# Kernel tuning notes

Measured on AMD Instinct MI355X. Metric: run time of the kernel, lower is better.

The kernel has to match this reference:

```python
import jax, jax.numpy as jnp
import numpy as np

D = 1024      # d_model
E = 8         # num_experts
K = 2         # top_k
H = 4096      # expert_dim (bottleneck)
P = 256       # proj_dim
BATCH, SEQ = 2, 2048
CLAMP_MAX = float(np.log(1.0 / 0.01))
INIT_T = 0.5


def setup_inputs() -> dict:
    key = jax.random.key(0)
    ks = jax.random.split(key, 6)
    x = jax.random.normal(ks[0], (BATCH, SEQ, D), jnp.float32)
    # cosine projector (nn.Linear default init ~ U(-1/sqrt(D), 1/sqrt(D)))
    lim = 1.0 / np.sqrt(D)
    Wp = jax.random.uniform(ks[1], (P, D), jnp.float32, -lim, lim)
    bp = jnp.zeros((P,), jnp.float32)
    sim = 0.01 * jax.random.normal(ks[2], (P, E), jnp.float32)
    temp = jnp.full((1,), np.log(1.0 / INIT_T), jnp.float32)
    # RepAdapter 1x1 convs == linear layers; xavier_uniform, zero bias
    bA = float(np.sqrt(6.0 / (D + H)))
    A = jax.random.uniform(ks[3], (E, H, D), jnp.float32, -bA, bA)
    a_bias = jnp.zeros((E, H), jnp.float32)
    Bw = jax.random.uniform(ks[4], (E, D, H), jnp.float32, -bA, bA)
    b_bias = jnp.zeros((E, D), jnp.float32)
    return dict(x=x, Wp=Wp, bp=bp, sim=sim, temp=temp, A=A, a_bias=a_bias, Bw=Bw, b_bias=b_bias)


def reference(x, Wp, bp, sim, temp, A, a_bias, Bw, b_bias):
    B, S, d = x.shape
    e = sim.shape[1]
    xf = x.reshape(-1, d)                                  # [T, D]
    # cosine gate
    proj = xf @ Wp.T + bp                                  # [T, P]
    projn = proj / jnp.maximum(jnp.linalg.norm(proj, axis=1, keepdims=True), 1e-12)
    simn = sim / jnp.maximum(jnp.linalg.norm(sim, axis=0, keepdims=True), 1e-12)
    scale = jnp.exp(jnp.minimum(temp, CLAMP_MAX))          # [1]
    gate_probs = jax.nn.softmax((projn @ simn) * scale, axis=-1)   # [T, E]
    topv, topi = jax.lax.top_k(gate_probs, K)              # [T, K]
    topv = topv / (topv.sum(axis=-1, keepdims=True) + 1e-8)
    # per-token per-expert combine weight
    w = jnp.sum(topv[:, :, None] * jax.nn.one_hot(topi, e, dtype=x.dtype), axis=1)  # [T, E]

    # experts: y_e(x) = x + B_e(A_e x + a_e) + b_e (no nonlinearity); combine weighted
    def body(acc, params):
        Ae, ab, Be, bb, we = params
        h = xf @ Ae.T + ab                                 # [T, H]
        f = h @ Be.T + bb                                  # [T, D]
        return acc + we[:, None] * (xf + f), None

    out, _ = jax.lax.scan(body, jnp.zeros_like(xf), (A, a_bias, Bw, b_bias, w.T))
    out = out.reshape(B, S, d)

    frac = gate_probs.mean(axis=0)                         # expert_fractions
    aux_loss = jnp.sum((frac - 1.0 / e) ** 2)
    usage = jnp.bincount(topi.reshape(-1), length=e).astype(jnp.float32)
    return out, aux_loss, frac, usage
```

## Files before the change

kernel.cpp:

```cpp
#include <hip/hip_runtime.h>
#include <stdint.h>


typedef __attribute__((ext_vector_type(4))) float floatx4;
typedef __attribute__((ext_vector_type(8))) short shortx8;
typedef unsigned short ushort_t;

#define T_TOKENS 4096
#define D_DIM    1024
#define E_EXP    8
#define H_DIM    4096
#define P_DIM    256
#define ROWS_PAD 10240
#define MBLK     40
#define MBLK1    80

__device__ __forceinline__ ushort_t f2bf(float f) {
  union { float f; unsigned int u; } c; c.f = f;
  unsigned int u = c.u;
  unsigned int r = u + 0x7FFFu + ((u >> 16) & 1u);
  return (ushort_t)(r >> 16);
}

__device__ __forceinline__ void stage16(const ushort_t* g, ushort_t* l) {
  __builtin_amdgcn_global_load_lds((const __attribute__((address_space(1))) void*)g,
                                   (__attribute__((address_space(3))) void*)l, 16, 0, 0);
}

__global__ __launch_bounds__(256) void k_cvt2(const float* __restrict__ srcA,
                                              const float* __restrict__ srcB,
                                              ushort_t* __restrict__ dstA,
                                              ushort_t* __restrict__ dstB) {
  int g = blockIdx.x * 256 + threadIdx.x;
  const float* s; ushort_t* d; int i;
  if (g < 8388608) { s = srcA; d = dstA; i = g; }
  else             { s = srcB; d = dstB; i = g - 8388608; }
  floatx4 v = ((const floatx4*)s)[i];
  ushort4 o; o.x = f2bf(v.x); o.y = f2bf(v.y); o.z = f2bf(v.z); o.w = f2bf(v.w);
  ((ushort4*)d)[i] = o;
}

__global__ __launch_bounds__(256) void k_small_init(int* counts, int* cursor,
                                                    float* frac_sum, int* row2tok) {
  int g = blockIdx.x * 256 + threadIdx.x;
  if (g < 8) { counts[g] = 0; cursor[g] = 0; frac_sum[g] = 0.f; }
  if (g < ROWS_PAD) row2tok[g] = -1;
}

__global__ __launch_bounds__(256) void k_proj(const float* __restrict__ x,
                                              const float* __restrict__ Wp,
                                              const float* __restrict__ bp,
                                              float* __restrict__ proj) {
  __shared__ float Wc[256 * 36];
  __shared__ float Xc[16 * 36];
  int tid = threadIdx.x;
  int t0 = blockIdx.x * 16;
  int cg = tid & 31, tg = tid >> 5;
  floatx4 acc[2][8];
#pragma unroll
  for (int a = 0; a < 2; a++)
#pragma unroll
    for (int b = 0; b < 8; b++) acc[a][b] = (floatx4){0.f, 0.f, 0.f, 0.f};
  for (int kc = 0; kc < 32; ++kc) {
    int k0 = kc * 32;
    __syncthreads();
#pragma unroll
    for (int it = 0; it < 8; ++it) {
      int f = it * 256 + tid;
      int j = f >> 3, kk = (f & 7) << 2;
      floatx4 v = *(const floatx4*)(Wp + j * 1024 + k0 + kk);
      *(floatx4*)(Wc + j * 36 + kk) = v;
    }
    if (tid < 128) {
      int t = tid >> 3, kk = (tid & 7) << 2;
      floatx4 v = *(const floatx4*)(x + (size_t)(t0 + t) * 1024 + k0 + kk);
      *(floatx4*)(Xc + t * 36 + kk) = v;
    }
    __syncthreads();
#pragma unroll
    for (int k4 = 0; k4 < 8; ++k4) {
      floatx4 xv[2], wv[8];
#pragma unroll
      for (int tt = 0; tt < 2; tt++) xv[tt] = *(floatx4*)(Xc + (tg * 2 + tt) * 36 + k4 * 4);
#pragma unroll
      for (int jj = 0; jj < 8; jj++) wv[jj] = *(floatx4*)(Wc + (cg + jj * 32) * 36 + k4 * 4);
#pragma unroll
      for (int tt = 0; tt < 2; tt++)
#pragma unroll
        for (int jj = 0; jj < 8; jj++) acc[tt][jj] += xv[tt] * wv[jj];
    }
  }
#pragma unroll
  for (int tt = 0; tt < 2; tt++)
#pragma unroll
    for (int jj = 0; jj < 8; jj++) {
      floatx4 a = acc[tt][jj];
      float s = (a.x + a.y) + (a.z + a.w);
      int t = t0 + tg * 2 + tt, j = cg + jj * 32;
      proj[t * 256 + j] = s + bp[j];
    }
}

__global__ __launch_bounds__(128) void k_gate(const float* __restrict__ proj,
                                              const float* __restrict__ sim,
                                              const float* __restrict__ temp,
                                              int* __restrict__ topi, float* __restrict__ wslot,
                                              float* __restrict__ swsum,
                                              float* __restrict__ frac_sum, int* __restrict__ counts) {
  __shared__ float simT[8][256];
  __shared__ float snorm[8];
  __shared__ float fracs[8];
  __shared__ int cnts[8];
  int tid = threadIdx.x;
  for (int i = tid; i < 2048; i += 128) { int p = i >> 3, e = i & 7; simT[e][p] = sim[i]; }
  if (tid < 8) { fracs[tid] = 0.f; cnts[tid] = 0; }
  __syncthreads();
  if (tid < 8) {
    float s = 0.f;
    for (int p = 0; p < 256; p++) { float v = simT[tid][p]; s += v * v; }
    snorm[tid] = fmaxf(sqrtf(s), 1e-12f);
  }
  __syncthreads();
  int t = blockIdx.x * 128 + tid;
  floatx4 n4 = (floatx4){0.f, 0.f, 0.f, 0.f};
  floatx4 d4[8];
#pragma unroll
  for (int e = 0; e < 8; e++) d4[e] = (floatx4){0.f, 0.f, 0.f, 0.f};
  const floatx4* pr = (const floatx4*)(proj + t * 256);
  for (int k4 = 0; k4 < 64; ++k4) {
    floatx4 p = pr[k4];
    n4 += p * p;
#pragma unroll
    for (int e = 0; e < 8; e++) d4[e] += p * *(const floatx4*)(&simT[e][k4 * 4]);
  }
  float nrm = fmaxf(sqrtf((n4.x + n4.y) + (n4.z + n4.w)), 1e-12f);
  float scale = expf(fminf(temp[0], 4.6051701859880914f));
  float pe[8];
  float mx = -1e30f;
#pragma unroll
  for (int e = 0; e < 8; e++) {
    float d = (d4[e].x + d4[e].y) + (d4[e].z + d4[e].w);
    pe[e] = d / (nrm * snorm[e]) * scale;
    mx = fmaxf(mx, pe[e]);
  }
  float sum = 0.f;
#pragma unroll
  for (int e = 0; e < 8; e++) { pe[e] = expf(pe[e] - mx); sum += pe[e]; }
#pragma unroll
  for (int e = 0; e < 8; e++) pe[e] /= sum;
  int i0 = 0;
#pragma unroll
  for (int e = 1; e < 8; e++) if (pe[e] > pe[i0]) i0 = e;
  int i1 = (i0 == 0) ? 1 : 0;
#pragma unroll
  for (int e = 0; e < 8; e++) if (e != i1 && e != i0 && pe[e] > pe[i1]) i1 = e;
  float v0 = pe[i0], v1 = pe[i1];
  float s2 = v0 + v1 + 1e-8f;
  float w0 = v0 / s2, w1 = v1 / s2;
  topi[t * 2] = i0; topi[t * 2 + 1] = i1;
  wslot[t * 2] = w0; wslot[t * 2 + 1] = w1;
  swsum[t] = w0 + w1;
#pragma unroll
  for (int e = 0; e < 8; e++) atomicAdd(&fracs[e], pe[e]);
  atomicAdd(&cnts[i0], 1); atomicAdd(&cnts[i1], 1);
  __syncthreads();
  if (tid < 8) { atomicAdd(&frac_sum[tid], fracs[tid]); atomicAdd(&counts[tid], cnts[tid]); }
}

__global__ void k_scan(const int* __restrict__ counts, const float* __restrict__ frac_sum,
                       int* __restrict__ offsets, int* __restrict__ blk2e,
                       float* __restrict__ out_tail) {
  __shared__ int offs[9];
  if (threadIdx.x == 0) {
    int off = 0;
    for (int e = 0; e < 8; e++) { offs[e] = off; off += ((counts[e] + 255) >> 8) << 8; }
    offs[8] = off;
    for (int e = 0; e < 9; e++) offsets[e] = offs[e];
    float aux = 0.f;
    for (int e = 0; e < 8; e++) { float fr = frac_sum[e] / 4096.f; aux += (fr - 0.125f) * (fr - 0.125f); }
    out_tail[0] = aux;
  }
  __syncthreads();
  int tid = threadIdx.x;
  if (tid < MBLK) {
    int r = tid * 256, e = -1;
    for (int q = 0; q < 8; q++) if (r >= offs[q] && r < offs[q + 1]) e = q;
    blk2e[tid] = e;
  }
  if (tid < 8) {
    out_tail[1 + tid] = frac_sum[tid] / 4096.f;
    out_tail[9 + tid] = (float)counts[tid];
  }
}

__global__ __launch_bounds__(256) void k_assign(const int* __restrict__ topi,
                                                const float* __restrict__ wslot,
                                                const int* __restrict__ offsets,
                                                int* __restrict__ cursor,
                                                int* __restrict__ row2tok, float* __restrict__ roww) {
  int g = blockIdx.x * 256 + threadIdx.x;
  if (g >= 8192) return;
  int t = g >> 1;
  int e = topi[g];
  int pos = atomicAdd(&cursor[e], 1);
  int r = offsets[e] + pos;
  row2tok[r] = t;
  roww[r] = wslot[g];
}

__global__ __launch_bounds__(256) void k_gather(const float* __restrict__ x,
                                                const int* __restrict__ row2tok,
                                                ushort_t* __restrict__ xg) {
  int r = blockIdx.x * 4 + (threadIdx.x >> 6);
  int l = threadIdx.x & 63;
  int t = row2tok[r];
  ushort4* dst = (ushort4*)(xg + (size_t)r * 1024);
  if (t < 0) {
    ushort4 z; z.x = z.y = z.z = z.w = 0;
    for (int i = l; i < 256; i += 64) dst[i] = z;
  } else {
    const floatx4* src = (const floatx4*)(x + (size_t)t * 1024);
    for (int i = l; i < 256; i += 64) {
      floatx4 v = src[i];
      ushort4 o; o.x = f2bf(v.x); o.y = f2bf(v.y); o.z = f2bf(v.z); o.w = f2bf(v.w);
      dst[i] = o;
    }
  }
}

__global__ __launch_bounds__(256) void k_init_out(const float* __restrict__ x,
                                                  const float* __restrict__ swsum,
                                                  float* __restrict__ out) {
  int g = blockIdx.x * 256 + threadIdx.x;
  float s = swsum[g >> 8];
  floatx4 v = ((const floatx4*)x)[g];
  ((floatx4*)out)[g] = v * s;
}

__global__ __launch_bounds__(256, 2) void k_gemm1(const ushort_t* __restrict__ Aop0,
                                                  const ushort_t* __restrict__ Wall,
                                                  const float* __restrict__ bias,
                                                  const int* __restrict__ blk2e,
                                                  ushort_t* __restrict__ hout) {
  const int K = 1024, N = 4096;
  int gx = gridDim.x;
  int nwg = gx * gridDim.y;
  int flat = blockIdx.y * gx + blockIdx.x;
  int qq = nwg >> 3, rr = nwg & 7;
  int xcd = flat & 7, idx = flat >> 3;
  int swz = (xcd < rr ? xcd * (qq + 1) : rr * (qq + 1) + (xcd - rr) * qq) + idx;
  int rb = swz / gx, nb = swz - rb * gx;
  int e = blk2e[rb >> 1];
  if (e < 0) return;
  const ushort_t* Aop = Aop0 + (size_t)rb * 128 * K;
  const ushort_t* Bop = Wall + (size_t)e * N * K + (size_t)nb * 128 * K;

  __shared__ ushort_t As[2][8192], Bs[2][8192];

  int tid = threadIdx.x, lane = tid & 63, wv = tid >> 6;
  int l15 = lane & 15, q = lane >> 4;
  int wm = (wv & 1) << 6, wn = (wv >> 1) << 6;
  floatx4 acc[4][4];
#pragma unroll
  for (int i = 0; i < 4; i++)
#pragma unroll
    for (int j = 0; j < 4; j++) acc[i][j] = (floatx4){0.f, 0.f, 0.f, 0.f};

  int srow = tid >> 3, schunk = tid & 7;

  auto stage = [&](int kt, int buf) {
#pragma unroll
    for (int r = 0; r < 4; ++r) {
      int row = (r << 5) + srow;
      size_t goff = (size_t)row * K + (size_t)(kt << 6) + (size_t)((schunk ^ (row & 7)) << 3);
      int loff = ((r << 8) + (wv << 6)) << 3;
      stage16(Aop + goff, &As[buf][loff]);
      stage16(Bop + goff, &Bs[buf][loff]);
    }
  };

  stage(0, 0);
  __syncthreads();
  int cur = 0;
  for (int kt = 0; kt < 16; ++kt) {
    if (kt + 1 < 16) stage(kt + 1, cur ^ 1);
    const ushort_t* Ab = As[cur];
    const ushort_t* Bb = Bs[cur];
#pragma unroll
    for (int kc = 0; kc < 2; ++kc) {
      int cw = (kc << 2) + q;
      shortx8 af[4], bfv[4];
#pragma unroll
      for (int i = 0; i < 4; ++i) {
        int row = wm + i * 16 + l15;
        af[i] = *(const shortx8*)(Ab + (row << 6) + ((cw ^ (row & 7)) << 3));
      }
#pragma unroll
      for (int j = 0; j < 4; ++j) {
        int row = wn + j * 16 + l15;
        bfv[j] = *(const shortx8*)(Bb + (row << 6) + ((cw ^ (row & 7)) << 3));
      }
#pragma unroll
      for (int i = 0; i < 4; ++i)
#pragma unroll
        for (int j = 0; j < 4; ++j)
          acc[i][j] = __builtin_amdgcn_mfma_f32_16x16x32_bf16(af[i], bfv[j], acc[i][j], 0, 0, 0);
    }
    __syncthreads();
    cur ^= 1;
  }

  const float* be = bias + (size_t)e * N + (size_t)nb * 128;
  ushort_t* hp = hout + (size_t)(rb * 128) * N + (size_t)nb * 128;
#pragma unroll
  for (int j = 0; j < 4; ++j) {
    int n = wn + j * 16 + l15;
    float bv = be[n];
#pragma unroll
    for (int i = 0; i < 4; ++i)
#pragma unroll
      for (int r = 0; r < 4; ++r) {
        int m = wm + i * 16 + (q << 2) + r;
        hp[(size_t)m * N + n] = f2bf(acc[i][j][r] + bv);
      }
  }
}

__global__ __launch_bounds__(256, 4) void k_gemm2(const ushort_t* __restrict__ Aop0,
                                                  const ushort_t* __restrict__ Wall,
                                                  const float* __restrict__ bias,
                                                  const int* __restrict__ blk2e,
                                                  int K, int N,
                                                  float* __restrict__ outp,
                                                  const int* __restrict__ row2tok,
                                                  const float* __restrict__ roww) {
  int gx = gridDim.x;
  int nwg = gx * gridDim.y;
  int flat = blockIdx.y * gx + blockIdx.x;
  int qq = nwg >> 3, rr = nwg & 7;
  int xcd = flat & 7, idx = flat >> 3;
  int swz = (xcd < rr ? xcd * (qq + 1) : rr * (qq + 1) + (xcd - rr) * qq) + idx;
  int rb = swz / gx, nb = swz - rb * gx;

  int e = blk2e[rb >> 1];
  if (e < 0) return;
  int Kslice = K / gridDim.z;
  int kbase = blockIdx.z * Kslice;
  const ushort_t* Aop = Aop0 + (size_t)rb * 128 * K + kbase;
  const ushort_t* Bop = Wall + (size_t)e * N * K + (size_t)nb * 128 * K + kbase;

  __shared__ ushort_t As[8192], Bs[8192];

  int tid = threadIdx.x, lane = tid & 63, wv = tid >> 6;
  int l15 = lane & 15, q = lane >> 4;
  int wm = (wv & 1) << 6, wn = (wv >> 1) << 6;
  floatx4 acc[4][4];
#pragma unroll
  for (int i = 0; i < 4; i++)
#pragma unroll
    for (int j = 0; j < 4; j++) acc[i][j] = (floatx4){0.f, 0.f, 0.f, 0.f};

  int srow = tid >> 3, schunk = tid & 7;
  int ksteps = Kslice >> 6;

  for (int kt = 0; kt < ksteps; ++kt) {
#pragma unroll
    for (int r = 0; r < 4; ++r) {
      int row = (r << 5) + srow;
      size_t goff = (size_t)row * K + (size_t)(kt << 6) + (size_t)((schunk ^ (row & 7)) << 3);
      int loff = ((r << 8) + (wv << 6)) << 3;
      stage16(Aop + goff, &As[loff]);
      stage16(Bop + goff, &Bs[loff]);
    }
    __syncthreads();
#pragma unroll
    for (int kc = 0; kc < 2; ++kc) {
      int cw = (kc << 2) + q;
      shortx8 af[4], bfv[4];
#pragma unroll
      for (int i = 0; i < 4; ++i) {
        int row = wm + i * 16 + l15;
        af[i] = *(const shortx8*)(As + (row << 6) + ((cw ^ (row & 7)) << 3));
      }
#pragma unroll
      for (int j = 0; j < 4; ++j) {
        int row = wn + j * 16 + l15;
        bfv[j] = *(const shortx8*)(Bs + (row << 6) + ((cw ^ (row & 7)) << 3));
      }
#pragma unroll
      for (int i = 0; i < 4; ++i)
#pragma unroll
        for (int j = 0; j < 4; ++j)
          acc[i][j] = __builtin_amdgcn_mfma_f32_16x16x32_bf16(af[i], bfv[j], acc[i][j], 0, 0, 0);
    }
    __syncthreads();
  }

  const float* be = bias + (size_t)e * N + (size_t)nb * 128;
  bool addb = (blockIdx.z == 0);
#pragma unroll
  for (int j = 0; j < 4; ++j) {
    int n = wn + j * 16 + l15;
    float bv = addb ? be[n] : 0.f;
#pragma unroll
    for (int i = 0; i < 4; ++i)
#pragma unroll
      for (int r = 0; r < 4; ++r) {
        int m = wm + i * 16 + (q << 2) + r;
        int grow = rb * 128 + m;
        int tok = row2tok[grow];
        if (tok < 0) continue;
        float w = roww[grow];
        atomicAdd(outp + (size_t)tok * 1024 + (size_t)nb * 128 + n, (acc[i][j][r] + bv) * w);
      }
  }
}

extern "C" void kernel_launch(void* const* d_in, const int* in_sizes, int n_in,
                              void* d_out, int out_size, void* d_ws, size_t ws_size,
                              hipStream_t stream) {
  (void)in_sizes; (void)n_in; (void)out_size; (void)ws_size;
  const float* x      = (const float*)d_in[0];
  const float* Wp     = (const float*)d_in[1];
  const float* bp     = (const float*)d_in[2];
  const float* sim    = (const float*)d_in[3];
  const float* temp   = (const float*)d_in[4];
  const float* A      = (const float*)d_in[5];
  const float* a_bias = (const float*)d_in[6];
  const float* Bw     = (const float*)d_in[7];
  const float* b_bias = (const float*)d_in[8];
  float* out = (float*)d_out;

  char* ws = (char*)d_ws;
  ushort_t* Abf    = (ushort_t*)(ws);
  ushort_t* Bbf    = (ushort_t*)(ws + 67108864);
  ushort_t* xg     = (ushort_t*)(ws + 134217728);
  ushort_t* h      = (ushort_t*)(ws + 155189248);
  float*    proj   = (float*)   (ws + 239075328);
  int*      topi   = (int*)     (ws + 243269632);
  float*    wslot  = (float*)   (ws + 243302400);
  float*    swsum  = (float*)   (ws + 243335168);
  int*      row2tok= (int*)     (ws + 243351552);
  float*    roww   = (float*)   (ws + 243392512);
  int*      counts = (int*)     (ws + 243433472);
  int*      cursor = (int*)     (ws + 243433504);
  int*      offsets= (int*)     (ws + 243433536);
  int*      blk2e  = (int*)     (ws + 243433600);
  float*    fracs  = (float*)   (ws + 243433760);

  k_cvt2<<<65536, 256, 0, stream>>>(A, Bw, Abf, Bbf);
  k_small_init<<<40, 256, 0, stream>>>(counts, cursor, fracs, row2tok);
  k_proj<<<256, 256, 0, stream>>>(x, Wp, bp, proj);
  k_gate<<<32, 128, 0, stream>>>(proj, sim, temp, topi, wslot, swsum, fracs, counts);
  k_scan<<<1, 128, 0, stream>>>(counts, fracs, offsets, blk2e, out + 4194304);
  k_assign<<<32, 256, 0, stream>>>(topi, wslot, offsets, cursor, row2tok, roww);
  k_gather<<<ROWS_PAD / 4, 256, 0, stream>>>(x, row2tok, xg);
  k_init_out<<<4096, 256, 0, stream>>>(x, swsum, out);
  k_gemm1<<<dim3(32, MBLK1, 1), 256, 0, stream>>>(xg, Abf, a_bias, blk2e, h);
  k_gemm2<<<dim3(8, MBLK1, 2), 256, 0, stream>>>(h, Bbf, b_bias, blk2e, 4096, 1024,
                                                 out, row2tok, roww);
}
```

Measured before the change: 736.5 us.

## Fuse gather and output init into token scatter; single-buffer gemm1 LDS

Replaces the per-row gather kernel and the separate output-init kernel with one per-token scatter kernel. It reads each x row once, writes the scaled residual to out, and writes the bf16 copy to both assigned expert rows using a new tok2row map filled by k_assign. gemm1 drops LDS double buffering to a single buffer with a sync after each stage, so launch bounds can rise to 5 waves per EU; gemm2's launch bounds are raised to 5 as well. The trade-off is that gemm1 loses load/compute overlap in exchange for more resident blocks, and padded xg rows are no longer zeroed.

```diff
diff --git a/kernel.cpp b/kernel.cpp
--- a/kernel.cpp
+++ b/kernel.cpp
@@ -197,7 +197,8 @@
                                                 const float* __restrict__ wslot,
                                                 const int* __restrict__ offsets,
                                                 int* __restrict__ cursor,
-                                                int* __restrict__ row2tok, float* __restrict__ roww) {
+                                                int* __restrict__ row2tok, float* __restrict__ roww,
+                                                int* __restrict__ tok2row) {
   int g = blockIdx.x * 256 + threadIdx.x;
   if (g >= 8192) return;
   int t = g >> 1;
@@ -206,38 +207,25 @@
   int r = offsets[e] + pos;
   row2tok[r] = t;
   roww[r] = wslot[g];
-}
-
-__global__ __launch_bounds__(256) void k_gather(const float* __restrict__ x,
-                                                const int* __restrict__ row2tok,
-                                                ushort_t* __restrict__ xg) {
-  int r = blockIdx.x * 4 + (threadIdx.x >> 6);
-  int l = threadIdx.x & 63;
-  int t = row2tok[r];
-  ushort4* dst = (ushort4*)(xg + (size_t)r * 1024);
-  if (t < 0) {
-    ushort4 z; z.x = z.y = z.z = z.w = 0;
-    for (int i = l; i < 256; i += 64) dst[i] = z;
-  } else {
-    const floatx4* src = (const floatx4*)(x + (size_t)t * 1024);
-    for (int i = l; i < 256; i += 64) {
-      floatx4 v = src[i];
-      ushort4 o; o.x = f2bf(v.x); o.y = f2bf(v.y); o.z = f2bf(v.z); o.w = f2bf(v.w);
-      dst[i] = o;
-    }
-  }
-}
-
-__global__ __launch_bounds__(256) void k_init_out(const float* __restrict__ x,
-                                                  const float* __restrict__ swsum,
-                                                  float* __restrict__ out) {
-  int g = blockIdx.x * 256 + threadIdx.x;
-  float s = swsum[g >> 8];
-  floatx4 v = ((const floatx4*)x)[g];
-  ((floatx4*)out)[g] = v * s;
-}
-
-__global__ __launch_bounds__(256, 2) void k_gemm1(const ushort_t* __restrict__ Aop0,
+  tok2row[g] = r;
+}
+
+__global__ __launch_bounds__(256) void k_scatter(const float* __restrict__ x,
+                                                 const float* __restrict__ swsum,
+                                                 const int* __restrict__ tok2row,
+                                                 float* __restrict__ out,
+                                                 ushort_t* __restrict__ xg) {
+  int t = blockIdx.x, tid = threadIdx.x;
+  float s = swsum[t];
+  floatx4 v = ((const floatx4*)(x + (size_t)t * 1024))[tid];
+  ((floatx4*)(out + (size_t)t * 1024))[tid] = v * s;
+  ushort4 o; o.x = f2bf(v.x); o.y = f2bf(v.y); o.z = f2bf(v.z); o.w = f2bf(v.w);
+  int r0 = tok2row[t * 2], r1 = tok2row[t * 2 + 1];
+  ((ushort4*)(xg + (size_t)r0 * 1024))[tid] = o;
+  ((ushort4*)(xg + (size_t)r1 * 1024))[tid] = o;
+}
+
+__global__ __launch_bounds__(256, 5) void k_gemm1(const ushort_t* __restrict__ Aop0,
                                                   const ushort_t* __restrict__ Wall,
                                                   const float* __restrict__ bias,
                                                   const int* __restrict__ blk2e,
@@ -255,7 +243,7 @@
   const ushort_t* Aop = Aop0 + (size_t)rb * 128 * K;
   const ushort_t* Bop = Wall + (size_t)e * N * K + (size_t)nb * 128 * K;
 
-  __shared__ ushort_t As[2][8192], Bs[2][8192];
+  __shared__ ushort_t As[8192], Bs[8192];
 
   int tid = threadIdx.x, lane = tid & 63, wv = tid >> 6;
   int l15 = lane & 15, q = lane >> 4;
@@ -268,24 +256,16 @@
 
   int srow = tid >> 3, schunk = tid & 7;
 
-  auto stage = [&](int kt, int buf) {
+  for (int kt = 0; kt < 16; ++kt) {
 #pragma unroll
     for (int r = 0; r < 4; ++r) {
       int row = (r << 5) + srow;
       size_t goff = (size_t)row * K + (size_t)(kt << 6) + (size_t)((schunk ^ (row & 7)) << 3);
       int loff = ((r << 8) + (wv << 6)) << 3;
-      stage16(Aop + goff, &As[buf][loff]);
-      stage16(Bop + goff, &Bs[buf][loff]);
-    }
-  };
-
-  stage(0, 0);
-  __syncthreads();
-  int cur = 0;
-  for (int kt = 0; kt < 16; ++kt) {
-    if (kt + 1 < 16) stage(kt + 1, cur ^ 1);
-    const ushort_t* Ab = As[cur];
-    const ushort_t* Bb = Bs[cur];
+      stage16(Aop + goff, &As[loff]);
+      stage16(Bop + goff, &Bs[loff]);
+    }
+    __syncthreads();
 #pragma unroll
     for (int kc = 0; kc < 2; ++kc) {
       int cw = (kc << 2) + q;
@@ -293,12 +273,12 @@
 #pragma unroll
       for (int i = 0; i < 4; ++i) {
         int row = wm + i * 16 + l15;
-        af[i] = *(const shortx8*)(Ab + (row << 6) + ((cw ^ (row & 7)) << 3));
+        af[i] = *(const shortx8*)(As + (row << 6) + ((cw ^ (row & 7)) << 3));
       }
 #pragma unroll
       for (int j = 0; j < 4; ++j) {
         int row = wn + j * 16 + l15;
-        bfv[j] = *(const shortx8*)(Bb + (row << 6) + ((cw ^ (row & 7)) << 3));
+        bfv[j] = *(const shortx8*)(Bs + (row << 6) + ((cw ^ (row & 7)) << 3));
       }
 #pragma unroll
       for (int i = 0; i < 4; ++i)
@@ -307,7 +287,6 @@
           acc[i][j] = __builtin_amdgcn_mfma_f32_16x16x32_bf16(af[i], bfv[j], acc[i][j], 0, 0, 0);
     }
     __syncthreads();
-    cur ^= 1;
   }
 
   const float* be = bias + (size_t)e * N + (size_t)nb * 128;
@@ -326,7 +305,7 @@
   }
 }
 
-__global__ __launch_bounds__(256, 4) void k_gemm2(const ushort_t* __restrict__ Aop0,
+__global__ __launch_bounds__(256, 5) void k_gemm2(const ushort_t* __restrict__ Aop0,
                                                   const ushort_t* __restrict__ Wall,
                                                   const float* __restrict__ bias,
                                                   const int* __restrict__ blk2e,
@@ -437,6 +416,7 @@
   ushort_t* xg     = (ushort_t*)(ws + 134217728);
   ushort_t* h      = (ushort_t*)(ws + 155189248);
   float*    proj   = (float*)   (ws + 239075328);
+  int*      tok2row= (int*)     (ws + 239075328);
   int*      topi   = (int*)     (ws + 243269632);
   float*    wslot  = (float*)   (ws + 243302400);
   float*    swsum  = (float*)   (ws + 243335168);
@@ -453,9 +433,8 @@
   k_proj<<<256, 256, 0, stream>>>(x, Wp, bp, proj);
   k_gate<<<32, 128, 0, stream>>>(proj, sim, temp, topi, wslot, swsum, fracs, counts);
   k_scan<<<1, 128, 0, stream>>>(counts, fracs, offsets, blk2e, out + 4194304);
-  k_assign<<<32, 256, 0, stream>>>(topi, wslot, offsets, cursor, row2tok, roww);
-  k_gather<<<ROWS_PAD / 4, 256, 0, stream>>>(x, row2tok, xg);
-  k_init_out<<<4096, 256, 0, stream>>>(x, swsum, out);
+  k_assign<<<32, 256, 0, stream>>>(topi, wslot, offsets, cursor, row2tok, roww, tok2row);
+  k_scatter<<<4096, 256, 0, stream>>>(x, swsum, tok2row, out, xg);
   k_gemm1<<<dim3(32, MBLK1, 1), 256, 0, stream>>>(xg, Abf, a_bias, blk2e, h);
   k_gemm2<<<dim3(8, MBLK1, 2), 256, 0, stream>>>(h, Bbf, b_bias, blk2e, 4096, 1024,
                                                  out, row2tok, roww);
```

Measured after the change: 973.2 us. 1.32x slower.
